# Optimization experiments

Measured on AMD Instinct MI355X. Metric: run time of the kernel, lower is better.

Reference implementation:

```python
import jax, jax.numpy as jnp
import numpy as np
import math

HEAD = 4
D_MODEL = 128
N_NODES = 2048
SEQ_LEN = 1
D_K = D_MODEL // HEAD
BATCH = 64


def conv1x1_relu(x, w, b):
    # x: [B, C, N, L], w: [O, C], b: [O]  (1x1 Conv2d + ReLU; dropout is identity in eval)
    return jax.nn.relu(jnp.einsum('oc,bcnl->bonl', w, x) + b[None, :, None, None])


def setup_inputs() -> dict:
    key = jax.random.key(0)
    ks = jax.random.split(key, 12)
    s = 0.05
    return {
        'x': jax.random.normal(ks[0], (BATCH, D_MODEL, N_NODES, SEQ_LEN), jnp.float32),
        'q_w': jax.random.normal(ks[1], (D_MODEL, D_MODEL), jnp.float32) * s,
        'q_b': jnp.zeros((D_MODEL,), jnp.float32),
        'v_w': jax.random.normal(ks[2], (D_MODEL, D_MODEL), jnp.float32) * s,
        'v_b': jnp.zeros((D_MODEL,), jnp.float32),
        'c_w': jax.random.normal(ks[3], (D_MODEL, D_MODEL), jnp.float32) * s,
        'c_b': jnp.zeros((D_MODEL,), jnp.float32),
        'memory': jax.random.normal(ks[4], (HEAD, SEQ_LEN, N_NODES, D_K), jnp.float32) * s,
        'nodevec1': jax.random.normal(ks[5], (N_NODES, 10), jnp.float32),
        'nodevec2': jax.random.normal(ks[6], (10, N_NODES), jnp.float32),
        'weights_pool': jax.random.normal(ks[7], (SEQ_LEN, 3, 3), jnp.float32) * s,
        'bias_pool': jax.random.normal(ks[8], (N_NODES, D_K), jnp.float32) * s,
        'aff_w': jnp.ones((D_MODEL, N_NODES, SEQ_LEN), jnp.float32),
        'aff_b': jnp.zeros((D_MODEL, N_NODES, SEQ_LEN), jnp.float32),
    }


def reference(x, q_w, q_b, v_w, v_b, c_w, c_b, memory, nodevec1, nodevec2,
              weights_pool, bias_pool, aff_w, aff_b):
    B = x.shape[0]
    scale = math.sqrt(D_K)

    query = conv1x1_relu(x, q_w, q_b)
    value = conv1x1_relu(x, v_w, v_b)

    # [B, d_model, N, L] -> [B, h, d_k, N, L] -> [B, h, L, N, d_k]
    def split_heads(t):
        return t.reshape(B, HEAD, D_K, N_NODES, SEQ_LEN).transpose(0, 1, 4, 3, 2)

    query = split_heads(query)
    value = split_heads(value)

    key_ = jax.nn.softmax(memory / scale, axis=-1)      # [h, L, N, d_k]
    query = jax.nn.softmax(query / scale, axis=-1)      # [B, h, L, N, d_k]

    Aapt = jax.nn.softmax(jax.nn.relu(nodevec1 @ nodevec2), axis=-1)  # [N, N]

    kv = jnp.einsum('hlnx,bhlny->bhlxy', key_, value)          # [B,h,L,d_k,d_k]
    attn_qkv = jnp.einsum('bhlnx,bhlxy->bhlny', query, kv)     # [B,h,L,N,d_k]

    weights = jnp.einsum('nm,dio->nio', Aapt, weights_pool)    # [N,3,3]
    bias_dyn = Aapt @ bias_pool                                # [N,d_k]
    attn_dyn = jnp.einsum('bhlnc,nio->bhlnc', value, weights) + bias_dyn[None, None, None, :, :]

    out = attn_qkv + attn_dyn                                  # [B,h,L,N,d_k]
    out = out.transpose(0, 1, 4, 3, 2).reshape(B, D_MODEL, N_NODES, SEQ_LEN)
    out = conv1x1_relu(out, c_w, c_b)

    # num_nodes (2048) not in [170, 358, 5] -> affine-residual branch runs
    out = out * aff_w[None] + aff_b[None] + out
    return out
```

## Files before the change

kernel.cpp:

```cpp
#include <hip/hip_runtime.h>

#define NB 64
#define CH 128
#define NNODE 2048
#define NH 4
#define DKK 32
#define INVS 0.17677669529663687f

typedef __bf16 bf16x8 __attribute__((ext_vector_type(8)));
typedef float f32x4 __attribute__((ext_vector_type(4)));
typedef unsigned short ushort_t;

union U16x8 { uint4 u; bf16x8 b; unsigned short s[8]; };
union U16x4 { uint2 u; unsigned short s[4]; };

__device__ inline bf16x8 as_bf16x8(uint4 u){ U16x8 x; x.u = u; return x.b; }
__device__ inline unsigned short f2b(float f){ __bf16 h = (__bf16)f; return __builtin_bit_cast(unsigned short, h); }
__device__ inline float b2f(unsigned short u){ __bf16 h = __builtin_bit_cast(__bf16, u); return (float)h; }

#define XT_IDX(n, c) ((n) * 136 + ((c) ^ ((((n) >> 2) & 7) << 3)))

__global__ __launch_bounds__(256) void kA(const float* __restrict__ qw,
    const float* __restrict__ vw, const float* __restrict__ cw,
    const float* __restrict__ memory, const float* __restrict__ bias_pool,
    ushort_t* __restrict__ wqb, ushort_t* __restrict__ wvb, ushort_t* __restrict__ wcb,
    ushort_t* __restrict__ keysT, float* __restrict__ bias_dyn,
    ushort_t* __restrict__ bpT,
    const float* __restrict__ nv1, const float* __restrict__ nv2,
    ushort_t* __restrict__ Ebuf)
{
  __shared__ float red[4];
  int tid = threadIdx.x;
  if (blockIdx.x < 256) {
    int gid = blockIdx.x * 256 + tid;
    if (gid < 16384) { wqb[gid] = f2b(qw[gid]); wvb[gid] = f2b(vw[gid]); wcb[gid] = f2b(cw[gid]); }
    bias_dyn[gid] = 0.f;
    { int k = gid >> 11, m = gid & 2047;
      bpT[gid] = f2b(bias_pool[m * 32 + k]); }
    if (gid < 8192) {
      int h = gid >> 11, n = gid & 2047;
      const float* src = memory + (size_t)gid * 32;
      float v[32]; float m = -1e30f;
      #pragma unroll
      for (int i = 0; i < 32; ++i) { v[i] = src[i] * INVS; m = fmaxf(m, v[i]); }
      float s = 0.f;
      #pragma unroll
      for (int i = 0; i < 32; ++i) { v[i] = __expf(v[i] - m); s += v[i]; }
      float inv = 1.f / s;
      #pragma unroll
      for (int i = 0; i < 32; ++i)
        keysT[(size_t)(h * 32 + i) * 2048 + n] = f2b(v[i] * inv);
    }
  } else {
    int n = blockIdx.x - 256;
    float a1[10];
    #pragma unroll
    for (int d = 0; d < 10; ++d) a1[d] = nv1[n * 10 + d];
    int m0 = tid * 8;
    float s[8];
    #pragma unroll
    for (int j = 0; j < 8; ++j) s[j] = 0.f;
    #pragma unroll
    for (int d = 0; d < 10; ++d) {
      const float* p = nv2 + d * 2048 + m0;
      float4 u = *(const float4*)p; float4 v = *(const float4*)(p + 4);
      s[0] += a1[d] * u.x; s[1] += a1[d] * u.y; s[2] += a1[d] * u.z; s[3] += a1[d] * u.w;
      s[4] += a1[d] * v.x; s[5] += a1[d] * v.y; s[6] += a1[d] * v.z; s[7] += a1[d] * v.w;
    }
    float e[8]; float sum = 0.f;
    #pragma unroll
    for (int j = 0; j < 8; ++j) { e[j] = __expf(fmaxf(s[j], 0.f)); sum += e[j]; }
    #pragma unroll
    for (int d = 1; d < 64; d <<= 1) sum += __shfl_xor(sum, d);
    if ((tid & 63) == 0) red[tid >> 6] = sum;
    __syncthreads();
    float inv = 1.f / (red[0] + red[1] + red[2] + red[3]);
    U16x8 o;
    #pragma unroll
    for (int j = 0; j < 8; ++j) o.s[j] = f2b(e[j] * inv);
    *(uint4*)(Ebuf + (size_t)n * 2048 + m0) = o.u;
  }
}

__global__ __launch_bounds__(256, 4) void kB(
    const ushort_t* __restrict__ Ebuf, const ushort_t* __restrict__ bpT,
    float* __restrict__ bias_dyn,
    const float* __restrict__ x,
    const ushort_t* __restrict__ wqb, const ushort_t* __restrict__ wvb,
    const float* __restrict__ qbias, const float* __restrict__ vbias,
    const ushort_t* __restrict__ keysT,
    ushort_t* __restrict__ QsT, ushort_t* __restrict__ VT,
    float* __restrict__ kvp)
{
  __shared__ __align__(16) ushort_t XT[64 * 136];
  __shared__ __align__(16) ushort_t QO[64][136];
  int tid = threadIdx.x; int wv = tid >> 6; int lane = tid & 63;
  int quad = lane >> 4; int l16 = lane & 15;
  f32x4 zero4 = {0.f,0.f,0.f,0.f};

  if (blockIdx.x < 128) {
    int bid = blockIdx.x;
    int n0 = (bid >> 3) * 128;
    int m0 = (bid & 7) * 256;
    int r0 = n0 + 32 * wv;
    f32x4 acc[2][2];
    acc[0][0] = zero4; acc[0][1] = zero4; acc[1][0] = zero4; acc[1][1] = zero4;
    for (int ks = 0; ks < 256; ks += 32) {
      int mb = m0 + ks + 8 * quad;
      bf16x8 a0 = *(const bf16x8*)(Ebuf + (size_t)(r0 + l16) * 2048 + mb);
      bf16x8 a1 = *(const bf16x8*)(Ebuf + (size_t)(r0 + 16 + l16) * 2048 + mb);
      bf16x8 b0 = *(const bf16x8*)(bpT + (size_t)l16 * 2048 + mb);
      bf16x8 b1 = *(const bf16x8*)(bpT + (size_t)(16 + l16) * 2048 + mb);
      acc[0][0] = __builtin_amdgcn_mfma_f32_16x16x32_bf16(a0, b0, acc[0][0], 0, 0, 0);
      acc[0][1] = __builtin_amdgcn_mfma_f32_16x16x32_bf16(a0, b1, acc[0][1], 0, 0, 0);
      acc[1][0] = __builtin_amdgcn_mfma_f32_16x16x32_bf16(a1, b0, acc[1][0], 0, 0, 0);
      acc[1][1] = __builtin_amdgcn_mfma_f32_16x16x32_bf16(a1, b1, acc[1][1], 0, 0, 0);
    }
    #pragma unroll
    for (int rt = 0; rt < 2; ++rt)
      #pragma unroll
      for (int ct = 0; ct < 2; ++ct)
        #pragma unroll
        for (int r = 0; r < 4; ++r)
          atomicAdd(bias_dyn + (size_t)(r0 + 16*rt + 4*quad + r) * 32 + 16*ct + l16,
                    acc[rt][ct][r]);
    return;
  }

  int bid = blockIdx.x - 128; int b = bid >> 5; int n0 = (bid & 31) * 64;

  uint4 wq[2][4];
  #pragma unroll
  for (int ct = 0; ct < 2; ++ct)
    #pragma unroll
    for (int k0 = 0; k0 < 4; ++k0)
      wq[ct][k0] = *(const uint4*)(wqb + (32 * wv + 16 * ct + l16) * 128 + 32 * k0 + 8 * quad);

  {
    float4 r[8];
    int n4 = 4 * (tid & 15);
    #pragma unroll
    for (int p = 0; p < 2; ++p) {
      int c4 = 4 * ((tid >> 4) + 16 * p);
      #pragma unroll
      for (int j = 0; j < 4; ++j)
        r[4 * p + j] = *(const float4*)(x + (size_t)(b * 128 + c4 + j) * 2048 + n0 + n4);
    }
    #pragma unroll
    for (int p = 0; p < 2; ++p) {
      int c4 = 4 * ((tid >> 4) + 16 * p);
      #pragma unroll
      for (int i = 0; i < 4; ++i) {
        U16x4 w;
        w.s[0] = f2b(((const float*)&r[4 * p + 0])[i]);
        w.s[1] = f2b(((const float*)&r[4 * p + 1])[i]);
        w.s[2] = f2b(((const float*)&r[4 * p + 2])[i]);
        w.s[3] = f2b(((const float*)&r[4 * p + 3])[i]);
        *(uint2*)&XT[XT_IDX(n4 + i, c4)] = w.u;
      }
    }
  }
  __syncthreads();

  {
    float4 qb4[2];
    #pragma unroll
    for (int ct = 0; ct < 2; ++ct)
      qb4[ct] = *(const float4*)(qbias + 32 * wv + 16 * ct + 4 * quad);
    #pragma unroll
    for (int nt = 0; nt < 4; ++nt) {
      f32x4 aq[2]; aq[0] = zero4; aq[1] = zero4;
      #pragma unroll
      for (int k0 = 0; k0 < 4; ++k0) {
        bf16x8 bfrag = *(const bf16x8*)&XT[XT_IDX(16 * nt + l16, 32 * k0 + 8 * quad)];
        aq[0] = __builtin_amdgcn_mfma_f32_16x16x32_bf16(as_bf16x8(wq[0][k0]), bfrag, aq[0], 0, 0, 0);
        aq[1] = __builtin_amdgcn_mfma_f32_16x16x32_bf16(as_bf16x8(wq[1][k0]), bfrag, aq[1], 0, 0, 0);
      }
      float sq[2][4]; float sum = 0.f;
      #pragma unroll
      for (int ct = 0; ct < 2; ++ct)
        #pragma unroll
        for (int r = 0; r < 4; ++r) {
          sq[ct][r] = __expf(fmaxf(aq[ct][r] + ((const float*)&qb4[ct])[r], 0.f) * INVS);
          sum += sq[ct][r];
        }
      sum += __shfl_xor(sum, 16);
      sum += __shfl_xor(sum, 32);
      float inv = 1.f / sum;
      #pragma unroll
      for (int ct = 0; ct < 2; ++ct) {
        U16x4 w;
        #pragma unroll
        for (int r = 0; r < 4; ++r) w.s[r] = f2b(sq[ct][r] * inv);
        *(uint2*)&QO[16 * nt + l16][32 * wv + 16 * ct + 4 * quad] = w.u;
      }
    }
  }

  uint2 vout[4][2];
  {
    uint4 wvw[2][4];
    #pragma unroll
    for (int ct = 0; ct < 2; ++ct)
      #pragma unroll
      for (int k0 = 0; k0 < 4; ++k0)
        wvw[ct][k0] = *(const uint4*)(wvb + (32 * wv + 16 * ct + l16) * 128 + 32 * k0 + 8 * quad);
    float4 vb4[2];
    #pragma unroll
    for (int ct = 0; ct < 2; ++ct)
      vb4[ct] = *(const float4*)(vbias + 32 * wv + 16 * ct + 4 * quad);
    #pragma unroll
    for (int nt = 0; nt < 4; ++nt) {
      f32x4 av[2]; av[0] = zero4; av[1] = zero4;
      #pragma unroll
      for (int k0 = 0; k0 < 4; ++k0) {
        bf16x8 bfrag = *(const bf16x8*)&XT[XT_IDX(16 * nt + l16, 32 * k0 + 8 * quad)];
        av[0] = __builtin_amdgcn_mfma_f32_16x16x32_bf16(as_bf16x8(wvw[0][k0]), bfrag, av[0], 0, 0, 0);
        av[1] = __builtin_amdgcn_mfma_f32_16x16x32_bf16(as_bf16x8(wvw[1][k0]), bfrag, av[1], 0, 0, 0);
      }
      #pragma unroll
      for (int ct = 0; ct < 2; ++ct) {
        U16x4 w;
        #pragma unroll
        for (int r = 0; r < 4; ++r)
          w.s[r] = f2b(fmaxf(av[ct][r] + ((const float*)&vb4[ct])[r], 0.f));
        vout[nt][ct] = w.u;
      }
    }
  }
  __syncthreads();

  #pragma unroll
  for (int nt = 0; nt < 4; ++nt)
    #pragma unroll
    for (int ct = 0; ct < 2; ++ct)
      *(uint2*)&XT[XT_IDX(16 * nt + l16, 32 * wv + 16 * ct + 4 * quad)] = vout[nt][ct];
  __syncthreads();

  {
    f32x4 akv[2][2];
    akv[0][0] = zero4; akv[0][1] = zero4; akv[1][0] = zero4; akv[1][1] = zero4;
    #pragma unroll
    for (int ks = 0; ks < 2; ++ks) {
      const ushort_t* kp = keysT + (size_t)(32 * wv) * 2048 + n0 + 32 * ks + 8 * quad;
      bf16x8 ka0 = *(const bf16x8*)(kp + (size_t)l16 * 2048);
      bf16x8 ka1 = *(const bf16x8*)(kp + (size_t)(16 + l16) * 2048);
      U16x8 v0, v1;
      #pragma unroll
      for (int j = 0; j < 8; ++j) {
        int rowk = 32 * ks + 8 * quad + j;
        v0.s[j] = XT[XT_IDX(rowk, 32 * wv + l16)];
        v1.s[j] = XT[XT_IDX(rowk, 32 * wv + 16 + l16)];
      }
      akv[0][0] = __builtin_amdgcn_mfma_f32_16x16x32_bf16(ka0, v0.b, akv[0][0], 0, 0, 0);
      akv[0][1] = __builtin_amdgcn_mfma_f32_16x16x32_bf16(ka0, v1.b, akv[0][1], 0, 0, 0);
      akv[1][0] = __builtin_amdgcn_mfma_f32_16x16x32_bf16(ka1, v0.b, akv[1][0], 0, 0, 0);
      akv[1][1] = __builtin_amdgcn_mfma_f32_16x16x32_bf16(ka1, v1.b, akv[1][1], 0, 0, 0);
    }
    float* kdst = kvp + (size_t)bid * 4096 + wv * 1024;
    #pragma unroll
    for (int xt = 0; xt < 2; ++xt)
      #pragma unroll
      for (int yt = 0; yt < 2; ++yt)
        #pragma unroll
        for (int r = 0; r < 4; ++r)
          kdst[(16 * yt + l16) * 32 + 16 * xt + 4 * quad + r] = akv[xt][yt][r];
  }

  #pragma unroll
  for (int j = 0; j < 4; ++j) {
    int id = tid + 256 * j; int n = id >> 4; int u = id & 15;
    size_t go = (size_t)(b * 2048 + n0 + n) * 128 + 8 * u;
    *(uint4*)(QsT + go) = *(uint4*)&QO[n][8 * u];
    *(uint4*)(VT  + go) = *(uint4*)&XT[XT_IDX(n, 8 * u)];
  }
}

__global__ __launch_bounds__(256) void kred(const float* __restrict__ kvp,
    float* __restrict__ kvws)
{
  int gid = blockIdx.x * 256 + threadIdx.x;
  int b = gid >> 10; int i = gid & 1023;
  const float* p = kvp + (size_t)(b * 32) * 4096 + i * 4;
  float4 s = {0.f,0.f,0.f,0.f};
  #pragma unroll
  for (int t = 0; t < 32; ++t) {
    float4 v = *(const float4*)(p + (size_t)t * 4096);
    s.x += v.x; s.y += v.y; s.z += v.z; s.w += v.w;
  }
  *(float4*)(kvws + (size_t)gid * 4) = s;
}

__global__ __launch_bounds__(256, 3) void k3_out(const ushort_t* __restrict__ QsT,
    const ushort_t* __restrict__ VT, const float* __restrict__ kvws,
    const float* __restrict__ bias_dyn, const ushort_t* __restrict__ wcb,
    const float* __restrict__ cbias, const float* __restrict__ wpool,
    const float* __restrict__ aff_w, const float* __restrict__ aff_b,
    float* __restrict__ out)
{
  int bid = blockIdx.x; int b = bid >> 5; int n0 = (bid & 31) * 64;
  int tid = threadIdx.x; int wv = tid >> 6; int lane = tid & 63;
  int quad = lane >> 4; int l16 = lane & 15;
  __shared__ __align__(16) char smem[53760];
  ushort_t (*kvT)[32][40] = (ushort_t(*)[32][40])(smem);
  ushort_t (*MID)[136]    = (ushort_t(*)[136])(smem + 10240);
  ushort_t (*VL)[132]     = (ushort_t(*)[132])(smem + 27648);
  float    (*BD)[36]      = (float(*)[36])(smem + 44544);
  float    (*OST)[64]     = (float(*)[64])(smem + 10240);

  float Ws = 0.f;
  #pragma unroll
  for (int i = 0; i < 9; ++i) Ws += wpool[i];

  uint4 wc[2][4];
  #pragma unroll
  for (int mt = 0; mt < 2; ++mt)
    #pragma unroll
    for (int k0 = 0; k0 < 4; ++k0)
      wc[mt][k0] = *(const uint4*)(wcb + (32 * wv + 16 * mt + l16) * 128 + 32 * k0 + 8 * quad);

  #pragma unroll
  for (int p = 0; p < 16; ++p) {
    int id = tid + 256 * p;
    kvT[id >> 10][(id >> 5) & 31][id & 31] = f2b(kvws[(size_t)b * 4096 + id]);
  }
  #pragma unroll
  for (int p = 0; p < 4; ++p) {
    int id = tid + 256 * p; int n = id >> 4; int u = id & 15;
    *(uint4*)&VL[n][8 * u] = *(const uint4*)(VT + (size_t)(b * 2048 + n0 + n) * 128 + 8 * u);
  }
  #pragma unroll
  for (int p = 0; p < 2; ++p) {
    int id = tid + 256 * p; int n = id >> 3; int g = id & 7;
    *(float4*)&BD[n][4 * g] = *(const float4*)(bias_dyn + (size_t)(n0 + n) * 32 + 4 * g);
  }
  __syncthreads();

  f32x4 zero4 = {0.f,0.f,0.f,0.f};
  f32x4 acc1[4][2];
  #pragma unroll
  for (int nt = 0; nt < 4; ++nt) { acc1[nt][0] = zero4; acc1[nt][1] = zero4; }
  #pragma unroll
  for (int nt = 0; nt < 4; ++nt) {
    bf16x8 aq = *(const bf16x8*)(QsT + (size_t)(b * 2048 + n0 + 16 * nt + l16) * 128 + 32 * wv + 8 * quad);
    #pragma unroll
    for (int ct = 0; ct < 2; ++ct)
      acc1[nt][ct] = __builtin_amdgcn_mfma_f32_16x16x32_bf16(
          aq, *(const bf16x8*)&kvT[wv][16 * ct + l16][8 * quad], acc1[nt][ct], 0, 0, 0);
  }

  #pragma unroll
  for (int nt = 0; nt < 4; ++nt)
    #pragma unroll
    for (int ct = 0; ct < 2; ++ct)
      #pragma unroll
      for (int r = 0; r < 4; ++r) {
        int nl = 16 * nt + 4 * quad + r;
        int cc = 32 * wv + 16 * ct + l16;
        float v = b2f(VL[nl][cc]);
        float bd = BD[nl][16 * ct + l16];
        MID[nl][cc] = f2b(acc1[nt][ct][r] + Ws * v + bd);
      }
  __syncthreads();

  f32x4 acc2[2][4];
  #pragma unroll
  for (int mt = 0; mt < 2; ++mt)
    #pragma unroll
    for (int nt = 0; nt < 4; ++nt) acc2[mt][nt] = zero4;
  #pragma unroll
  for (int k0 = 0; k0 < 4; ++k0) {
    bf16x8 bb[4];
    #pragma unroll
    for (int nt = 0; nt < 4; ++nt)
      bb[nt] = *(const bf16x8*)&MID[16 * nt + l16][32 * k0 + 8 * quad];
    #pragma unroll
    for (int mt = 0; mt < 2; ++mt)
      #pragma unroll
      for (int nt = 0; nt < 4; ++nt)
        acc2[mt][nt] = __builtin_amdgcn_mfma_f32_16x16x32_bf16(
            as_bf16x8(wc[mt][k0]), bb[nt], acc2[mt][nt], 0, 0, 0);
  }
  __syncthreads();

  float4 cb4[2];
  #pragma unroll
  for (int mt = 0; mt < 2; ++mt)
    cb4[mt] = *(const float4*)(cbias + 32 * wv + 16 * mt + 4 * quad);
  #pragma unroll
  for (int mt = 0; mt < 2; ++mt)
    #pragma unroll
    for (int nt = 0; nt < 4; ++nt)
      #pragma unroll
      for (int r = 0; r < 4; ++r) {
        int c_out = 32 * wv + 16 * mt + 4 * quad + r;
        OST[c_out][16 * nt + l16] = fmaxf(acc2[mt][nt][r] + ((const float*)&cb4[mt])[r], 0.f);
      }
  __syncthreads();

  #pragma unroll
  for (int p = 0; p < 8; ++p) {
    int id = tid + 256 * p; int c = id >> 4; int g = id & 15;
    float4 y = *(const float4*)&OST[c][4 * g];
    size_t ai = (size_t)c * 2048 + n0 + 4 * g;
    float4 aw4 = *(const float4*)(aff_w + ai);
    float4 ab4 = *(const float4*)(aff_b + ai);
    float4 o;
    o.x = y.x * aw4.x + ab4.x + y.x;
    o.y = y.y * aw4.y + ab4.y + y.y;
    o.z = y.z * aw4.z + ab4.z + y.z;
    o.w = y.w * aw4.w + ab4.w + y.w;
    *(float4*)(out + (size_t)(b * 128 + c) * 2048 + n0 + 4 * g) = o;
  }
}

extern "C" void kernel_launch(void* const* d_in, const int* in_sizes, int n_in,
                              void* d_out, int out_size, void* d_ws, size_t ws_size,
                              hipStream_t stream)
{
  const float* x      = (const float*)d_in[0];
  const float* qw     = (const float*)d_in[1];
  const float* qb     = (const float*)d_in[2];
  const float* vw     = (const float*)d_in[3];
  const float* vb     = (const float*)d_in[4];
  const float* cw     = (const float*)d_in[5];
  const float* cb     = (const float*)d_in[6];
  const float* memory = (const float*)d_in[7];
  const float* nv1    = (const float*)d_in[8];
  const float* nv2    = (const float*)d_in[9];
  const float* wpool  = (const float*)d_in[10];
  const float* bpool  = (const float*)d_in[11];
  const float* aw     = (const float*)d_in[12];
  const float* ab     = (const float*)d_in[13];
  float* out = (float*)d_out;

  char* ws = (char*)d_ws;
  ushort_t* QsT      = (ushort_t*)(ws);
  ushort_t* VT       = (ushort_t*)(ws + 33554432);
  float*    kvws     = (float*)   (ws + 67108864);
  ushort_t* keysT    = (ushort_t*)(ws + 68157440);
  float*    bias_dyn = (float*)   (ws + 69206016);
  ushort_t* wqb      = (ushort_t*)(ws + 69468160);
  ushort_t* wvb      = (ushort_t*)(ws + 69500928);
  ushort_t* wcb      = (ushort_t*)(ws + 69533696);
  ushort_t* Ebuf     = (ushort_t*)(ws + 69566464);
  ushort_t* bpT      = (ushort_t*)(ws + 77955072);
  float*    kvp      = (float*)   (ws + 78086144);

  kA<<<2304, 256, 0, stream>>>(qw, vw, cw, memory, bpool, wqb, wvb, wcb,
                               keysT, bias_dyn, bpT, nv1, nv2, Ebuf);
  kB<<<2176, 256, 0, stream>>>(Ebuf, bpT, bias_dyn, x, wqb, wvb, qb, vb,
                               keysT, QsT, VT, kvp);
  kred<<<256, 256, 0, stream>>>(kvp, kvws);
  k3_out<<<2048, 256, 0, stream>>>(QsT, VT, kvws, bias_dyn, wcb, cb, wpool, aw, ab, out);
}
```

Before: 209.0 us.

## Shrink LDS footprint with XOR swizzle and register kv fragments to raise occupancy

Replaces padded LDS row strides (136/132) with unpadded 128-wide rows indexed through an XOR swizzle in both kB and k3_out, cutting shared memory per block. In k3_out the kv matrix is loaded straight from global into registers as MFMA B fragments instead of staged through LDS, and bias_dyn is held in LDS as bf16, so LDS drops from ~53KB to ~38KB. Launch bounds are raised (kB 4→5, k3_out 3→4 waves per EU) to exploit the smaller footprint. The tighter register budget may cause spills, and rounding bias_dyn to bf16 loses a little precision.

```diff
diff --git a/kernel.cpp b/kernel.cpp
--- a/kernel.cpp
+++ b/kernel.cpp
@@ -18,7 +18,7 @@
 __device__ inline unsigned short f2b(float f){ __bf16 h = (__bf16)f; return __builtin_bit_cast(unsigned short, h); }
 __device__ inline float b2f(unsigned short u){ __bf16 h = __builtin_bit_cast(__bf16, u); return (float)h; }
 
-#define XT_IDX(n, c) ((n) * 136 + ((c) ^ ((((n) >> 2) & 7) << 3)))
+#define SWZ_IDX(n, c) ((n) * 128 + ((c) ^ ((((n) >> 2) & 7) << 3)))
 
 __global__ __launch_bounds__(256) void kA(const float* __restrict__ qw,
     const float* __restrict__ vw, const float* __restrict__ cw,
@@ -82,7 +82,7 @@
   }
 }
 
-__global__ __launch_bounds__(256, 4) void kB(
+__global__ __launch_bounds__(256, 5) void kB(
     const ushort_t* __restrict__ Ebuf, const ushort_t* __restrict__ bpT,
     float* __restrict__ bias_dyn,
     const float* __restrict__ x,
@@ -92,8 +92,8 @@
     ushort_t* __restrict__ QsT, ushort_t* __restrict__ VT,
     float* __restrict__ kvp)
 {
-  __shared__ __align__(16) ushort_t XT[64 * 136];
-  __shared__ __align__(16) ushort_t QO[64][136];
+  __shared__ __align__(16) ushort_t XT[64 * 128];
+  __shared__ __align__(16) ushort_t QO[64 * 128];
   int tid = threadIdx.x; int wv = tid >> 6; int lane = tid & 63;
   int quad = lane >> 4; int l16 = lane & 15;
   f32x4 zero4 = {0.f,0.f,0.f,0.f};
@@ -156,7 +156,7 @@
         w.s[1] = f2b(((const float*)&r[4 * p + 1])[i]);
         w.s[2] = f2b(((const float*)&r[4 * p + 2])[i]);
         w.s[3] = f2b(((const float*)&r[4 * p + 3])[i]);
-        *(uint2*)&XT[XT_IDX(n4 + i, c4)] = w.u;
+        *(uint2*)&XT[SWZ_IDX(n4 + i, c4)] = w.u;
       }
     }
   }
@@ -172,7 +172,7 @@
       f32x4 aq[2]; aq[0] = zero4; aq[1] = zero4;
       #pragma unroll
       for (int k0 = 0; k0 < 4; ++k0) {
-        bf16x8 bfrag = *(const bf16x8*)&XT[XT_IDX(16 * nt + l16, 32 * k0 + 8 * quad)];
+        bf16x8 bfrag = *(const bf16x8*)&XT[SWZ_IDX(16 * nt + l16, 32 * k0 + 8 * quad)];
         aq[0] = __builtin_amdgcn_mfma_f32_16x16x32_bf16(as_bf16x8(wq[0][k0]), bfrag, aq[0], 0, 0, 0);
         aq[1] = __builtin_amdgcn_mfma_f32_16x16x32_bf16(as_bf16x8(wq[1][k0]), bfrag, aq[1], 0, 0, 0);
       }
@@ -192,7 +192,7 @@
         U16x4 w;
         #pragma unroll
         for (int r = 0; r < 4; ++r) w.s[r] = f2b(sq[ct][r] * inv);
-        *(uint2*)&QO[16 * nt + l16][32 * wv + 16 * ct + 4 * quad] = w.u;
+        *(uint2*)&QO[SWZ_IDX(16 * nt + l16, 32 * wv + 16 * ct + 4 * quad)] = w.u;
       }
     }
   }
@@ -214,7 +214,7 @@
       f32x4 av[2]; av[0] = zero4; av[1] = zero4;
       #pragma unroll
       for (int k0 = 0; k0 < 4; ++k0) {
-        bf16x8 bfrag = *(const bf16x8*)&XT[XT_IDX(16 * nt + l16, 32 * k0 + 8 * quad)];
+        bf16x8 bfrag = *(const bf16x8*)&XT[SWZ_IDX(16 * nt + l16, 32 * k0 + 8 * quad)];
         av[0] = __builtin_amdgcn_mfma_f32_16x16x32_bf16(as_bf16x8(wvw[0][k0]), bfrag, av[0], 0, 0, 0);
         av[1] = __builtin_amdgcn_mfma_f32_16x16x32_bf16(as_bf16x8(wvw[1][k0]), bfrag, av[1], 0, 0, 0);
       }
@@ -234,7 +234,7 @@
   for (int nt = 0; nt < 4; ++nt)
     #pragma unroll
     for (int ct = 0; ct < 2; ++ct)
-      *(uint2*)&XT[XT_IDX(16 * nt + l16, 32 * wv + 16 * ct + 4 * quad)] = vout[nt][ct];
+      *(uint2*)&XT[SWZ_IDX(16 * nt + l16, 32 * wv + 16 * ct + 4 * quad)] = vout[nt][ct];
   __syncthreads();
 
   {
@@ -249,8 +249,8 @@
       #pragma unroll
       for (int j = 0; j < 8; ++j) {
         int rowk = 32 * ks + 8 * quad + j;
-        v0.s[j] = XT[XT_IDX(rowk, 32 * wv + l16)];
-        v1.s[j] = XT[XT_IDX(rowk, 32 * wv + 16 + l16)];
+        v0.s[j] = XT[SWZ_IDX(rowk, 32 * wv + l16)];
+        v1.s[j] = XT[SWZ_IDX(rowk, 32 * wv + 16 + l16)];
       }
       akv[0][0] = __builtin_amdgcn_mfma_f32_16x16x32_bf16(ka0, v0.b, akv[0][0], 0, 0, 0);
       akv[0][1] = __builtin_amdgcn_mfma_f32_16x16x32_bf16(ka0, v1.b, akv[0][1], 0, 0, 0);
@@ -271,8 +271,8 @@
   for (int j = 0; j < 4; ++j) {
     int id = tid + 256 * j; int n = id >> 4; int u = id & 15;
     size_t go = (size_t)(b * 2048 + n0 + n) * 128 + 8 * u;
-    *(uint4*)(QsT + go) = *(uint4*)&QO[n][8 * u];
-    *(uint4*)(VT  + go) = *(uint4*)&XT[XT_IDX(n, 8 * u)];
+    *(uint4*)(QsT + go) = *(uint4*)&QO[SWZ_IDX(n, 8 * u)];
+    *(uint4*)(VT  + go) = *(uint4*)&XT[SWZ_IDX(n, 8 * u)];
   }
 }
 
@@ -291,7 +291,7 @@
   *(float4*)(kvws + (size_t)gid * 4) = s;
 }
 
-__global__ __launch_bounds__(256, 3) void k3_out(const ushort_t* __restrict__ QsT,
+__global__ __launch_bounds__(256, 4) void k3_out(const ushort_t* __restrict__ QsT,
     const ushort_t* __restrict__ VT, const float* __restrict__ kvws,
     const float* __restrict__ bias_dyn, const ushort_t* __restrict__ wcb,
     const float* __restrict__ cbias, const float* __restrict__ wpool,
@@ -301,16 +301,62 @@
   int bid = blockIdx.x; int b = bid >> 5; int n0 = (bid & 31) * 64;
   int tid = threadIdx.x; int wv = tid >> 6; int lane = tid & 63;
   int quad = lane >> 4; int l16 = lane & 15;
-  __shared__ __align__(16) char smem[53760];
-  ushort_t (*kvT)[32][40] = (ushort_t(*)[32][40])(smem);
-  ushort_t (*MID)[136]    = (ushort_t(*)[136])(smem + 10240);
-  ushort_t (*VL)[132]     = (ushort_t(*)[132])(smem + 27648);
-  float    (*BD)[36]      = (float(*)[36])(smem + 44544);
-  float    (*OST)[64]     = (float(*)[64])(smem + 10240);
+  __shared__ __align__(16) char smem[37888];
+  ushort_t* MID = (ushort_t*)smem;
+  ushort_t* VL  = (ushort_t*)(smem + 16384);
+  ushort_t (*BD)[40] = (ushort_t(*)[40])(smem + 32768);
+  float    (*OST)[64] = (float(*)[64])smem;
+
+  float4 kvlo[2], kvhi[2];
+  #pragma unroll
+  for (int ct = 0; ct < 2; ++ct) {
+    const float* kp = kvws + (size_t)b * 4096 + wv * 1024 + (16 * ct + l16) * 32 + 8 * quad;
+    kvlo[ct] = *(const float4*)kp;
+    kvhi[ct] = *(const float4*)(kp + 4);
+  }
+  uint4 aqv[4];
+  #pragma unroll
+  for (int nt = 0; nt < 4; ++nt)
+    aqv[nt] = *(const uint4*)(QsT + (size_t)(b * 2048 + n0 + 16 * nt + l16) * 128 + 32 * wv + 8 * quad);
 
   float Ws = 0.f;
   #pragma unroll
   for (int i = 0; i < 9; ++i) Ws += wpool[i];
+
+  #pragma unroll
+  for (int p = 0; p < 4; ++p) {
+    int id = tid + 256 * p; int n = id >> 4; int u = id & 15;
+    *(uint4*)&VL[SWZ_IDX(n, 8 * u)] =
+        *(const uint4*)(VT + (size_t)(b * 2048 + n0 + n) * 128 + 8 * u);
+  }
+  #pragma unroll
+  for (int p = 0; p < 2; ++p) {
+    int id = tid + 256 * p; int n = id >> 3; int g = id & 7;
+    float4 v = *(const float4*)(bias_dyn + (size_t)(n0 + n) * 32 + 4 * g);
+    U16x4 w;
+    w.s[0] = f2b(v.x); w.s[1] = f2b(v.y); w.s[2] = f2b(v.z); w.s[3] = f2b(v.w);
+    *(uint2*)&BD[n][4 * g] = w.u;
+  }
+  U16x8 kf[2];
+  #pragma unroll
+  for (int ct = 0; ct < 2; ++ct)
+    #pragma unroll
+    for (int j = 0; j < 4; ++j) {
+      kf[ct].s[j]     = f2b(((const float*)&kvlo[ct])[j]);
+      kf[ct].s[4 + j] = f2b(((const float*)&kvhi[ct])[j]);
+    }
+  __syncthreads();
+
+  f32x4 zero4 = {0.f,0.f,0.f,0.f};
+  f32x4 acc1[4][2];
+  #pragma unroll
+  for (int nt = 0; nt < 4; ++nt) { acc1[nt][0] = zero4; acc1[nt][1] = zero4; }
+  #pragma unroll
+  for (int nt = 0; nt < 4; ++nt)
+    #pragma unroll
+    for (int ct = 0; ct < 2; ++ct)
+      acc1[nt][ct] = __builtin_amdgcn_mfma_f32_16x16x32_bf16(
+          as_bf16x8(aqv[nt]), kf[ct].b, acc1[nt][ct], 0, 0, 0);
 
   uint4 wc[2][4];
   #pragma unroll
@@ -318,36 +364,6 @@
     #pragma unroll
     for (int k0 = 0; k0 < 4; ++k0)
       wc[mt][k0] = *(const uint4*)(wcb + (32 * wv + 16 * mt + l16) * 128 + 32 * k0 + 8 * quad);
-
-  #pragma unroll
-  for (int p = 0; p < 16; ++p) {
-    int id = tid + 256 * p;
-    kvT[id >> 10][(id >> 5) & 31][id & 31] = f2b(kvws[(size_t)b * 4096 + id]);
-  }
-  #pragma unroll
-  for (int p = 0; p < 4; ++p) {
-    int id = tid + 256 * p; int n = id >> 4; int u = id & 15;
-    *(uint4*)&VL[n][8 * u] = *(const uint4*)(VT + (size_t)(b * 2048 + n0 + n) * 128 + 8 * u);
-  }
-  #pragma unroll
-  for (int p = 0; p < 2; ++p) {
-    int id = tid + 256 * p; int n = id >> 3; int g = id & 7;
-    *(float4*)&BD[n][4 * g] = *(const float4*)(bias_dyn + (size_t)(n0 + n) * 32 + 4 * g);
-  }
-  __syncthreads();
-
-  f32x4 zero4 = {0.f,0.f,0.f,0.f};
-  f32x4 acc1[4][2];
-  #pragma unroll
-  for (int nt = 0; nt < 4; ++nt) { acc1[nt][0] = zero4; acc1[nt][1] = zero4; }
-  #pragma unroll
-  for (int nt = 0; nt < 4; ++nt) {
-    bf16x8 aq = *(const bf16x8*)(QsT + (size_t)(b * 2048 + n0 + 16 * nt + l16) * 128 + 32 * wv + 8 * quad);
-    #pragma unroll
-    for (int ct = 0; ct < 2; ++ct)
-      acc1[nt][ct] = __builtin_amdgcn_mfma_f32_16x16x32_bf16(
-          aq, *(const bf16x8*)&kvT[wv][16 * ct + l16][8 * quad], acc1[nt][ct], 0, 0, 0);
-  }
 
   #pragma unroll
   for (int nt = 0; nt < 4; ++nt)
@@ -357,9 +373,9 @@
       for (int r = 0; r < 4; ++r) {
         int nl = 16 * nt + 4 * quad + r;
         int cc = 32 * wv + 16 * ct + l16;
-        float v = b2f(VL[nl][cc]);
-        float bd = BD[nl][16 * ct + l16];
-        MID[nl][cc] = f2b(acc1[nt][ct][r] + Ws * v + bd);
+        float v = b2f(VL[SWZ_IDX(nl, cc)]);
+        float bd = b2f(BD[nl][16 * ct + l16]);
+        MID[SWZ_IDX(nl, cc)] = f2b(acc1[nt][ct][r] + Ws * v + bd);
       }
   __syncthreads();
 
@@ -373,7 +389,7 @@
     bf16x8 bb[4];
     #pragma unroll
     for (int nt = 0; nt < 4; ++nt)
-      bb[nt] = *(const bf16x8*)&MID[16 * nt + l16][32 * k0 + 8 * quad];
+      bb[nt] = *(const bf16x8*)&MID[SWZ_IDX(16 * nt + l16, 32 * k0 + 8 * quad)];
     #pragma unroll
     for (int mt = 0; mt < 2; ++mt)
       #pragma unroll
```

After: 207.5 us (median of 2 runs). Within noise of the previous version (-0.7%).
